# Performance work log

Measured on AMD Instinct MI355X. Metric: run time of the kernel, lower is better.

## Reference

```python
import jax, jax.numpy as jnp
import numpy as np

INPUT_SIZE = 32
HIDDEN_SIZE = 128
N_HEAD = 8
NER_NUMS = 8
D = INPUT_SIZE * NER_NUMS  # 256, attention feature dim per head


def setup_inputs() -> dict:
    key = jax.random.key(0)
    ks = jax.random.split(key, 10)
    B, S = 8, 2048
    x = jax.random.normal(ks[0], (B, S, D), dtype=jnp.float32)
    bi_lstm_o = jax.random.normal(ks[1], (B, S, 2 * HIDDEN_SIZE), dtype=jnp.float32)
    # per-head linear params, stacked on leading head axis (nn.init.normal_ -> std 1)
    Qw = jax.random.normal(ks[2], (N_HEAD, 2 * HIDDEN_SIZE, D), dtype=jnp.float32)
    Qb = jax.random.normal(ks[3], (N_HEAD, D), dtype=jnp.float32)
    Kw = jax.random.normal(ks[4], (N_HEAD, D, D), dtype=jnp.float32)
    Kb = jax.random.normal(ks[5], (N_HEAD, D), dtype=jnp.float32)
    Vw = jax.random.normal(ks[6], (N_HEAD, D, D), dtype=jnp.float32)
    Vb = jax.random.normal(ks[7], (N_HEAD, D), dtype=jnp.float32)
    Cw = jax.random.normal(ks[8], (N_HEAD * D, NER_NUMS), dtype=jnp.float32)
    Cb = jax.random.normal(ks[9], (NER_NUMS,), dtype=jnp.float32)
    return {"x": x, "bi_lstm_o": bi_lstm_o, "Qw": Qw, "Qb": Qb, "Kw": Kw,
            "Kb": Kb, "Vw": Vw, "Vb": Vb, "Cw": Cw, "Cb": Cb}


def reference(x, bi_lstm_o, Qw, Qb, Kw, Kb, Vw, Vb, Cw, Cb):
    # q from bi_lstm_o, k/v from x; all heads batched on axis h
    q = jnp.einsum('bsf,hfd->hbsd', bi_lstm_o, Qw) + Qb[:, None, None, :]
    k = jnp.einsum('bsf,hfd->hbsd', x, Kw) + Kb[:, None, None, :]
    v = jnp.einsum('bsf,hfd->hbsd', x, Vw) + Vb[:, None, None, :]
    scale = 1.0 / jnp.sqrt(jnp.float32(D))
    scores = jnp.einsum('hbsd,hbtd->hbst', q, k) * scale  # [H,B,S,S]
    attn = jax.nn.softmax(scores, axis=-1)
    o = jnp.einsum('hbst,hbtd->hbsd', attn, v)  # [H,B,S,D]
    B, S = x.shape[0], x.shape[1]
    concat = jnp.transpose(o, (1, 2, 0, 3)).reshape(B, S, N_HEAD * D)  # head order matches torch.cat
    return concat @ Cw + Cb
```

## Files before the change

kernel.cpp:

```cpp
#include <hip/hip_runtime.h>

#define H_ 8
#define B_ 8
#define S_ 2048
#define D_ 256

#define KSTRIDE 264
#define VSTRIDE 40

typedef __attribute__((ext_vector_type(8))) _Float16 half8;
typedef __attribute__((ext_vector_type(4))) _Float16 half4v;
typedef __attribute__((ext_vector_type(4))) float f32x4;

__device__ inline void split8(const float* __restrict__ p, half8& hv, half8& lv) {
  float4 a = *(const float4*)p, b = *(const float4*)(p + 4);
  hv[0] = (_Float16)a.x; hv[1] = (_Float16)a.y; hv[2] = (_Float16)a.z; hv[3] = (_Float16)a.w;
  hv[4] = (_Float16)b.x; hv[5] = (_Float16)b.y; hv[6] = (_Float16)b.z; hv[7] = (_Float16)b.w;
  lv[0] = (_Float16)(a.x - (float)hv[0]); lv[1] = (_Float16)(a.y - (float)hv[1]);
  lv[2] = (_Float16)(a.z - (float)hv[2]); lv[3] = (_Float16)(a.w - (float)hv[3]);
  lv[4] = (_Float16)(b.x - (float)hv[4]); lv[5] = (_Float16)(b.y - (float)hv[5]);
  lv[6] = (_Float16)(b.z - (float)hv[6]); lv[7] = (_Float16)(b.w - (float)hv[7]);
}

__global__ void split_w_kernel(const float* __restrict__ W,
                               _Float16* __restrict__ thi, _Float16* __restrict__ tlo) {
  __shared__ float t[64][65];
  const int h = blockIdx.z, f0 = blockIdx.x * 64, d0 = blockIdx.y * 64;
  const int col = threadIdx.x & 63, rg = threadIdx.x >> 6;
#pragma unroll
  for (int it = 0; it < 16; ++it) {
    int f = rg * 16 + it;
    t[f][col] = W[((size_t)h * 256 + f0 + f) * 256 + d0 + col];
  }
  __syncthreads();
#pragma unroll
  for (int it = 0; it < 16; ++it) {
    int d = rg * 16 + it;
    float v = t[col][d];
    _Float16 hv = (_Float16)v;
    size_t idx = ((size_t)h * 256 + d0 + d) * 256 + f0 + col;
    thi[idx] = hv;
    tlo[idx] = (_Float16)(v - (float)hv);
  }
}

__global__ void out_init_kernel(float* __restrict__ out, const float* __restrict__ Cb) {
  int i = blockIdx.x * blockDim.x + threadIdx.x;
  if (i < B_ * S_ * 8) out[i] = Cb[i & 7];
}

template <int VMODE>
__global__ __launch_bounds__(256, 2) void proj_kernel(
    const float* __restrict__ A,
    const _Float16* __restrict__ Whi, const _Float16* __restrict__ Wlo,
    const float* __restrict__ bias, float oscale, int h0,
    _Float16* __restrict__ Ohi, _Float16* __restrict__ Olo) {
  constexpr bool TMULT = (VMODE != 1);
  __shared__ _Float16 a_hi[128 * VSTRIDE] __attribute__((aligned(16)));
  __shared__ _Float16 b_hi[128 * VSTRIDE] __attribute__((aligned(16)));
  __shared__ _Float16 a_lo[TMULT ? 128 * VSTRIDE : 8] __attribute__((aligned(16)));
  __shared__ _Float16 b_lo[TMULT ? 128 * VSTRIDE : 8] __attribute__((aligned(16)));
  const int tid = threadIdx.x;
  const int w = tid >> 6, lane = tid & 63;
  const int quad = lane >> 4, l15 = lane & 15;
  const int hb = blockIdx.z, h = h0 + (hb >> 3), b = hb & 7;
  const int s0 = blockIdx.x * 128, d0 = blockIdx.y * 128;
  const int wr = w >> 1, wc = w & 1;
  const f32x4 fz = {0.f, 0.f, 0.f, 0.f};
  f32x4 acc[4][4];
#pragma unroll
  for (int i = 0; i < 4; ++i)
#pragma unroll
    for (int j = 0; j < 4; ++j) acc[i][j] = fz;
  const size_t arow0 = (size_t)b * S_ + s0;
  const size_t wrow0 = (size_t)h * 256 + d0;
  for (int kk = 0; kk < 8; ++kk) {
    const int f0 = kk * 32;
    __syncthreads();
#pragma unroll
    for (int i = 0; i < 2; ++i) {
      int cc = i * 256 + tid;
      int r = cc >> 2, ch = (cc & 3) * 8;
      half8 hv, lv;
      split8(A + (arow0 + r) * 256 + f0 + ch, hv, lv);
      *(half8*)&a_hi[r * VSTRIDE + ch] = hv;
      size_t woff = (wrow0 + r) * 256 + f0 + ch;
      *(half8*)&b_hi[r * VSTRIDE + ch] = *(const half8*)(Whi + woff);
      if (TMULT) {
        *(half8*)&a_lo[r * VSTRIDE + ch] = lv;
        *(half8*)&b_lo[r * VSTRIDE + ch] = *(const half8*)(Wlo + woff);
      }
    }
    __syncthreads();
    half8 afh[4], afl[4], bfh[4], bfl[4];
#pragma unroll
    for (int t = 0; t < 4; ++t) {
      int ar = wr * 64 + t * 16 + l15;
      afh[t] = *(const half8*)&a_hi[ar * VSTRIDE + quad * 8];
      int br = wc * 64 + t * 16 + l15;
      bfh[t] = *(const half8*)&b_hi[br * VSTRIDE + quad * 8];
      if (TMULT) {
        afl[t] = *(const half8*)&a_lo[ar * VSTRIDE + quad * 8];
        bfl[t] = *(const half8*)&b_lo[br * VSTRIDE + quad * 8];
      }
    }
#pragma unroll
    for (int rf = 0; rf < 4; ++rf)
#pragma unroll
      for (int cf = 0; cf < 4; ++cf) {
        acc[rf][cf] = __builtin_amdgcn_mfma_f32_16x16x32_f16(afh[rf], bfh[cf], acc[rf][cf], 0, 0, 0);
        if (TMULT) {
          acc[rf][cf] = __builtin_amdgcn_mfma_f32_16x16x32_f16(afh[rf], bfl[cf], acc[rf][cf], 0, 0, 0);
          acc[rf][cf] = __builtin_amdgcn_mfma_f32_16x16x32_f16(afl[rf], bfh[cf], acc[rf][cf], 0, 0, 0);
        }
      }
  }
#pragma unroll
  for (int rf = 0; rf < 4; ++rf) {
#pragma unroll
    for (int cf = 0; cf < 4; ++cf) {
      const int d = d0 + wc * 64 + cf * 16 + l15;
      const float bv = bias[h * 256 + d];
      if (VMODE != 1) {
#pragma unroll
        for (int r = 0; r < 4; ++r) {
          const int s = s0 + wr * 64 + rf * 16 + quad * 4 + r;
          float val = (acc[rf][cf][r] + bv) * oscale;
          _Float16 hvv = (_Float16)val;
          size_t idx = ((size_t)hb * S_ + s) * 256 + d;
          Ohi[idx] = hvv;
          if (VMODE == 0) Olo[idx] = (_Float16)(val - (float)hvv);
        }
      } else {
        half4v pack;
#pragma unroll
        for (int r = 0; r < 4; ++r) pack[r] = (_Float16)((acc[rf][cf][r] + bv) * oscale);
        size_t idx = ((size_t)hb * 256 + d) * S_ + s0 + wr * 64 + rf * 16 + quad * 4;
        *(half4v*)(Ohi + idx) = pack;
      }
    }
  }
}

__global__ __launch_bounds__(256, 2) void flash_kernel(
    const _Float16* __restrict__ qhi, const _Float16* __restrict__ qlo,
    const _Float16* __restrict__ khi,
    const _Float16* __restrict__ vt, const float* __restrict__ Cw,
    float* __restrict__ out, int h0) {
  __shared__ _Float16 khi_s[32 * KSTRIDE] __attribute__((aligned(16)));
  __shared__ _Float16 vt_s[256 * VSTRIDE] __attribute__((aligned(16)));
  __shared__ _Float16 p_s[4][16 * VSTRIDE] __attribute__((aligned(16)));
  const int tid = threadIdx.x, w = tid >> 6, lane = tid & 63;
  const int quad = lane >> 4, l15 = lane & 15;
  const int hb = blockIdx.y, h = h0 + (hb >> 3), b = hb & 7;
  const int qbase = blockIdx.x * 64;
  half8 qfh[8], qfl[8];
  {
    size_t qrow = (size_t)hb * S_ + qbase + w * 16 + l15;
    const _Float16* qh = qhi + qrow * 256 + quad * 8;
    const _Float16* ql = qlo + qrow * 256 + quad * 8;
#pragma unroll
    for (int ks = 0; ks < 8; ++ks) {
      qfh[ks] = *(const half8*)(qh + ks * 32);
      qfl[ks] = *(const half8*)(ql + ks * 32);
    }
  }
  const f32x4 fz = {0.f, 0.f, 0.f, 0.f};
  f32x4 o_acc[16];
#pragma unroll
  for (int df = 0; df < 16; ++df) o_acc[df] = fz;
  float m_r[4], l_r[4];
#pragma unroll
  for (int r = 0; r < 4; ++r) { m_r[r] = -3.0e38f; l_r[r] = 0.f; }

  for (int kt = 0; kt < 64; ++kt) {
    __syncthreads();
    {
      size_t kbase = ((size_t)hb * S_ + kt * 32) * 256;
#pragma unroll
      for (int i = 0; i < 4; ++i) {
        int cc = i * 256 + tid;
        int kr = cc >> 5, kch = (cc & 31) * 8;
        *(half8*)&khi_s[kr * KSTRIDE + kch] = *(const half8*)(khi + kbase + kr * 256 + kch);
        int vd = cc >> 2, vch = (cc & 3) * 8;
        size_t voff = ((size_t)hb * 256 + vd) * S_ + kt * 32 + vch;
        *(half8*)&vt_s[vd * VSTRIDE + vch] = *(const half8*)(vt + voff);
      }
    }
    __syncthreads();
    f32x4 sc0 = fz, sc1 = fz;
#pragma unroll
    for (int ks = 0; ks < 8; ++ks) {
      half8 bh0 = *(const half8*)&khi_s[(0 * 16 + l15) * KSTRIDE + ks * 32 + quad * 8];
      sc0 = __builtin_amdgcn_mfma_f32_16x16x32_f16(qfh[ks], bh0, sc0, 0, 0, 0);
      sc0 = __builtin_amdgcn_mfma_f32_16x16x32_f16(qfl[ks], bh0, sc0, 0, 0, 0);
      half8 bh1 = *(const half8*)&khi_s[(1 * 16 + l15) * KSTRIDE + ks * 32 + quad * 8];
      sc1 = __builtin_amdgcn_mfma_f32_16x16x32_f16(qfh[ks], bh1, sc1, 0, 0, 0);
      sc1 = __builtin_amdgcn_mfma_f32_16x16x32_f16(qfl[ks], bh1, sc1, 0, 0, 0);
    }
    float al[4], p0[4], p1[4];
#pragma unroll
    for (int r = 0; r < 4; ++r) {
      float v = fmaxf(sc0[r], sc1[r]);
      v = fmaxf(v, __shfl_xor(v, 1));
      v = fmaxf(v, __shfl_xor(v, 2));
      v = fmaxf(v, __shfl_xor(v, 4));
      v = fmaxf(v, __shfl_xor(v, 8));
      float mn = fmaxf(m_r[r], v);
      al[r] = __expf(m_r[r] - mn);
      m_r[r] = mn;
      p0[r] = __expf(sc0[r] - mn);
      p1[r] = __expf(sc1[r] - mn);
      float s = p0[r] + p1[r];
      s += __shfl_xor(s, 1);
      s += __shfl_xor(s, 2);
      s += __shfl_xor(s, 4);
      s += __shfl_xor(s, 8);
      l_r[r] = l_r[r] * al[r] + s;
    }
#pragma unroll
    for (int r = 0; r < 4; ++r) {
      p_s[w][(quad * 4 + r) * VSTRIDE + l15] = (_Float16)p0[r];
      p_s[w][(quad * 4 + r) * VSTRIDE + 16 + l15] = (_Float16)p1[r];
    }
#pragma unroll
    for (int df = 0; df < 16; ++df)
#pragma unroll
      for (int r = 0; r < 4; ++r) o_acc[df][r] *= al[r];
    __syncthreads();
    half8 pf = *(const half8*)&p_s[w][l15 * VSTRIDE + quad * 8];
#pragma unroll
    for (int df = 0; df < 16; ++df) {
      half8 vf = *(const half8*)&vt_s[(df * 16 + l15) * VSTRIDE + quad * 8];
      o_acc[df] = __builtin_amdgcn_mfma_f32_16x16x32_f16(pf, vf, o_acc[df], 0, 0, 0);
    }
  }
  float rcl[4];
#pragma unroll
  for (int r = 0; r < 4; ++r) rcl[r] = 1.0f / l_r[r];
  float part[32];
#pragma unroll
  for (int i = 0; i < 32; ++i) part[i] = 0.f;
#pragma unroll
  for (int df = 0; df < 16; ++df) {
    const float4* cwv = (const float4*)(Cw + ((size_t)h * 256 + df * 16 + l15) * 8);
    float4 c0 = cwv[0], c1 = cwv[1];
#pragma unroll
    for (int r = 0; r < 4; ++r) {
      float ov = o_acc[df][r] * rcl[r];
      part[r * 8 + 0] += ov * c0.x;
      part[r * 8 + 1] += ov * c0.y;
      part[r * 8 + 2] += ov * c0.z;
      part[r * 8 + 3] += ov * c0.w;
      part[r * 8 + 4] += ov * c1.x;
      part[r * 8 + 5] += ov * c1.y;
      part[r * 8 + 6] += ov * c1.z;
      part[r * 8 + 7] += ov * c1.w;
    }
  }
#pragma unroll
  for (int i = 0; i < 32; ++i) {
    float v = part[i];
    v += __shfl_xor(v, 1);
    v += __shfl_xor(v, 2);
    v += __shfl_xor(v, 4);
    v += __shfl_xor(v, 8);
    part[i] = v;
  }
  if (l15 == 0) {
#pragma unroll
    for (int r = 0; r < 4; ++r) {
      int s = qbase + w * 16 + quad * 4 + r;
#pragma unroll
      for (int j = 0; j < 8; ++j)
        atomicAdd(&out[((size_t)b * S_ + s) * 8 + j], part[r * 8 + j]);
    }
  }
}

extern "C" void kernel_launch(void* const* d_in, const int* in_sizes, int n_in,
                              void* d_out, int out_size, void* d_ws, size_t ws_size,
                              hipStream_t stream) {
  const float* x  = (const float*)d_in[0];
  const float* bo = (const float*)d_in[1];
  const float* Qw = (const float*)d_in[2];
  const float* Qb = (const float*)d_in[3];
  const float* Kw = (const float*)d_in[4];
  const float* Kb = (const float*)d_in[5];
  const float* Vw = (const float*)d_in[6];
  const float* Vb = (const float*)d_in[7];
  const float* Cw = (const float*)d_in[8];
  const float* Cb = (const float*)d_in[9];
  float* out = (float*)d_out;

  const size_t NW  = (size_t)H_ * 256 * 256;
  const size_t NHB = (size_t)B_ * S_ * 256;
  const size_t ALN = 256;
  auto pad = [](size_t b) { return (b + 255) & ~(size_t)255; };

  int HC = 8;
  while (HC > 1) {
    size_t need = 6 * pad(NW * 2) + 4 * pad((size_t)HC * NHB * 2) + ALN;
    if (need <= ws_size) break;
    HC >>= 1;
  }

  char* base = (char*)d_ws;
  size_t off = 0;
  auto carve = [&](size_t nelem) -> _Float16* {
    _Float16* p = (_Float16*)(base + off);
    off += pad(nelem * 2);
    return p;
  };
  _Float16* qwt_hi = carve(NW); _Float16* qwt_lo = carve(NW);
  _Float16* kwt_hi = carve(NW); _Float16* kwt_lo = carve(NW);
  _Float16* vwt_hi = carve(NW); _Float16* vwt_lo = carve(NW);
  const size_t NC = (size_t)HC * NHB;
  _Float16* q_hi = carve(NC); _Float16* q_lo = carve(NC);
  _Float16* k_hi = carve(NC);
  _Float16* v_t  = carve(NC);

  dim3 wg(4, 4, 8);
  split_w_kernel<<<wg, 256, 0, stream>>>(Qw, qwt_hi, qwt_lo);
  split_w_kernel<<<wg, 256, 0, stream>>>(Kw, kwt_hi, kwt_lo);
  split_w_kernel<<<wg, 256, 0, stream>>>(Vw, vwt_hi, vwt_lo);
  out_init_kernel<<<(B_ * S_ * 8) / 256, 256, 0, stream>>>(out, Cb);

  for (int h0 = 0; h0 < H_; h0 += HC) {
    dim3 pg(16, 2, HC * 8);
    proj_kernel<0><<<pg, 256, 0, stream>>>(bo, qwt_hi, qwt_lo, Qb, 0.0625f, h0, q_hi, q_lo);
    proj_kernel<2><<<pg, 256, 0, stream>>>(x, kwt_hi, kwt_lo, Kb, 1.0f, h0, k_hi, nullptr);
    proj_kernel<1><<<pg, 256, 0, stream>>>(x, vwt_hi, vwt_lo, Vb, 1.0f, h0, v_t, nullptr);
    dim3 fg(32, HC * 8);
    flash_kernel<<<fg, 256, 0, stream>>>(q_hi, q_lo, k_hi, v_t, Cw, out, h0);
  }
}
```

Measured before the change: 967.9 us.

## Split PV accumulation across warps by D-slice instead of query rows

The P·V product is repartitioned so each warp owns a 64-wide slice of the head dimension for all 64 query rows, rather than all 256 dims for its own 16 rows. Each warp now loads a quarter of the V tile and reads all four warps' P tiles, so the V fragment loaded from LDS is reused across four MFMAs. Rescale factors and final row normalisers are exchanged through shared memory. The Cw epilogue is reworked to match, with a cheaper cross-quad reduction before the atomics. This adds extra LDS traffic for P and alpha plus one more small barrier pattern.

```diff
diff --git a/kernel.cpp b/kernel.cpp
--- a/kernel.cpp
+++ b/kernel.cpp
@@ -150,6 +150,8 @@
   __shared__ _Float16 khi_s[32 * KSTRIDE] __attribute__((aligned(16)));
   __shared__ _Float16 vt_s[256 * VSTRIDE] __attribute__((aligned(16)));
   __shared__ _Float16 p_s[4][16 * VSTRIDE] __attribute__((aligned(16)));
+  __shared__ float al_s[64];
+  __shared__ float rl_s[64];
   const int tid = threadIdx.x, w = tid >> 6, lane = tid & 63;
   const int quad = lane >> 4, l15 = lane & 15;
   const int hb = blockIdx.y, h = h0 + (hb >> 3), b = hb & 7;
@@ -166,9 +168,11 @@
     }
   }
   const f32x4 fz = {0.f, 0.f, 0.f, 0.f};
-  f32x4 o_acc[16];
-#pragma unroll
-  for (int df = 0; df < 16; ++df) o_acc[df] = fz;
+  f32x4 o_acc[4][4];
+#pragma unroll
+  for (int i = 0; i < 4; ++i)
+#pragma unroll
+    for (int j = 0; j < 4; ++j) o_acc[i][j] = fz;
   float m_r[4], l_r[4];
 #pragma unroll
   for (int r = 0; r < 4; ++r) { m_r[r] = -3.0e38f; l_r[r] = 0.f; }
@@ -223,59 +227,72 @@
       p_s[w][(quad * 4 + r) * VSTRIDE + l15] = (_Float16)p0[r];
       p_s[w][(quad * 4 + r) * VSTRIDE + 16 + l15] = (_Float16)p1[r];
     }
-#pragma unroll
-    for (int df = 0; df < 16; ++df)
-#pragma unroll
-      for (int r = 0; r < 4; ++r) o_acc[df][r] *= al[r];
-    __syncthreads();
-    half8 pf = *(const half8*)&p_s[w][l15 * VSTRIDE + quad * 8];
-#pragma unroll
-    for (int df = 0; df < 16; ++df) {
-      half8 vf = *(const half8*)&vt_s[(df * 16 + l15) * VSTRIDE + quad * 8];
-      o_acc[df] = __builtin_amdgcn_mfma_f32_16x16x32_f16(pf, vf, o_acc[df], 0, 0, 0);
-    }
-  }
-  float rcl[4];
-#pragma unroll
-  for (int r = 0; r < 4; ++r) rcl[r] = 1.0f / l_r[r];
-  float part[32];
-#pragma unroll
-  for (int i = 0; i < 32; ++i) part[i] = 0.f;
-#pragma unroll
-  for (int df = 0; df < 16; ++df) {
-    const float4* cwv = (const float4*)(Cw + ((size_t)h * 256 + df * 16 + l15) * 8);
-    float4 c0 = cwv[0], c1 = cwv[1];
+    if (l15 == 0) {
+#pragma unroll
+      for (int r = 0; r < 4; ++r) al_s[w * 16 + quad * 4 + r] = al[r];
+    }
+    __syncthreads();
+    float al_t[4];
+#pragma unroll
+    for (int st = 0; st < 4; ++st) al_t[st] = al_s[st * 16 + l15];
+#pragma unroll
+    for (int dtl = 0; dtl < 4; ++dtl)
+#pragma unroll
+      for (int st = 0; st < 4; ++st)
+#pragma unroll
+        for (int c = 0; c < 4; ++c) o_acc[dtl][st][c] *= al_t[st];
+    half8 pf[4];
+#pragma unroll
+    for (int st = 0; st < 4; ++st)
+      pf[st] = *(const half8*)&p_s[st][l15 * VSTRIDE + quad * 8];
+#pragma unroll
+    for (int dtl = 0; dtl < 4; ++dtl) {
+      half8 vf = *(const half8*)&vt_s[(w * 64 + dtl * 16 + l15) * VSTRIDE + quad * 8];
+#pragma unroll
+      for (int st = 0; st < 4; ++st)
+        o_acc[dtl][st] = __builtin_amdgcn_mfma_f32_16x16x32_f16(vf, pf[st], o_acc[dtl][st], 0, 0, 0);
+    }
+  }
+  if (l15 == 0) {
+#pragma unroll
+    for (int r = 0; r < 4; ++r) rl_s[w * 16 + quad * 4 + r] = 1.0f / l_r[r];
+  }
+  __syncthreads();
+  float rl_t[4];
+#pragma unroll
+  for (int st = 0; st < 4; ++st) rl_t[st] = rl_s[st * 16 + l15];
+  float part[4][8];
+#pragma unroll
+  for (int st = 0; st < 4; ++st)
+#pragma unroll
+    for (int j = 0; j < 8; ++j) part[st][j] = 0.f;
+#pragma unroll
+  for (int dtl = 0; dtl < 4; ++dtl) {
 #pragma unroll
     for (int r = 0; r < 4; ++r) {
-      float ov = o_acc[df][r] * rcl[r];
-      part[r * 8 + 0] += ov * c0.x;
-      part[r * 8 + 1] += ov * c0.y;
-      part[r * 8 + 2] += ov * c0.z;
-      part[r * 8 + 3] += ov * c0.w;
-      part[r * 8 + 4] += ov * c1.x;
-      part[r * 8 + 5] += ov * c1.y;
-      part[r * 8 + 6] += ov * c1.z;
-      part[r * 8 + 7] += ov * c1.w;
-    }
-  }
-#pragma unroll
-  for (int i = 0; i < 32; ++i) {
-    float v = part[i];
-    v += __shfl_xor(v, 1);
-    v += __shfl_xor(v, 2);
-    v += __shfl_xor(v, 4);
-    v += __shfl_xor(v, 8);
-    part[i] = v;
-  }
-  if (l15 == 0) {
-#pragma unroll
-    for (int r = 0; r < 4; ++r) {
-      int s = qbase + w * 16 + quad * 4 + r;
-#pragma unroll
-      for (int j = 0; j < 8; ++j)
-        atomicAdd(&out[((size_t)b * S_ + s) * 8 + j], part[r * 8 + j]);
-    }
-  }
+      const int d = w * 64 + dtl * 16 + quad * 4 + r;
+      const float4* cwv = (const float4*)(Cw + ((size_t)h * 256 + d) * 8);
+      float4 c0 = cwv[0], c1 = cwv[1];
+#pragma unroll
+      for (int st = 0; st < 4; ++st) {
+        float ov = o_acc[dtl][st][r];
+        part[st][0] += ov * c0.x; part[st][1] += ov * c0.y;
+        part[st][2] += ov * c0.z; part[st][3] += ov * c0.w;
+        part[st][4] += ov * c1.x; part[st][5] += ov * c1.y;
+        part[st][6] += ov * c1.z; part[st][7] += ov * c1.w;
+      }
+    }
+  }
+#pragma unroll
+  for (int st = 0; st < 4; ++st)
+#pragma unroll
+    for (int j = 0; j < 8; ++j) {
+      float v = part[st][j] * rl_t[st];
+      v += __shfl_xor(v, 16);
+      v += __shfl_xor(v, 32);
+      if (quad == 0)
+        atomicAdd(&out[((size_t)b * S_ + qbase + st * 16 + l15) * 8 + j], v);
+    }
 }
 
 extern "C" void kernel_launch(void* const* d_in, const int* in_sizes, int n_in,
```

Measured after the change: 1.018 ms. 5.2% more time.
